# Kernel tuning notes

Measured on AMD Instinct MI355X. Metric: run time of the kernel, lower is better.

The kernel has to match this reference:

```python
import jax, jax.numpy as jnp
import numpy as np
from math import log

B, L, D = 2, 4096, 2048
H, Dh, C, KW = 16, 128, 64, 4
EPS = 1e-5
SCALE = 0.02


def setup_inputs() -> dict:
    key = jax.random.key(0)
    ks = jax.random.split(key, 16)
    rn = lambda k, shp, sc=SCALE: jax.random.normal(k, shp, jnp.float32) * sc
    # dt_bias built like the torch module
    dt = jnp.exp(jax.random.uniform(ks[7], (H,)) * (log(0.1) - log(0.001)) + log(0.001))
    dt = jnp.clip(dt, 0.0001, None)
    dt_bias = dt + jnp.log(-jnp.expm1(-dt))
    return {
        "x": jax.random.normal(ks[0], (B, L, D), jnp.float32),
        "Wq": rn(ks[1], (H * Dh, D)),
        "Wk": rn(ks[2], (H * Dh, D)),
        "Wv": rn(ks[3], (H * Dh, D)),
        "Wb": rn(ks[4], (H, D)),
        "Wa": rn(ks[5], (H, D)),
        "A_log": jnp.log(jax.random.uniform(ks[6], (H,), minval=0.01, maxval=16.0)),
        "dt_bias": dt_bias,
        "conv_q": rn(ks[8], (H * Dh, 1, KW), 0.2),
        "conv_k": rn(ks[9], (H * Dh, 1, KW), 0.2),
        "conv_v": rn(ks[10], (H * Dh, 1, KW), 0.2),
        "Wg": rn(ks[11], (H * Dh, D)),
        "norm_w": jnp.ones((Dh,), jnp.float32),
        "Wo": rn(ks[12], (D, H * Dh)),
        "S0": jnp.zeros((B, H, Dh, Dh), jnp.float32),
    }


def _causal_dwconv(x, w):
    # x: [B,L,Ch]; w: [Ch,1,KW] depthwise causal conv (left pad KW-1), then SiLU
    y = jax.lax.conv_general_dilated(
        x.transpose(0, 2, 1), w, (1,), [(KW - 1, 0)],
        feature_group_count=w.shape[0], dimension_numbers=("NCH", "OIH", "NCH"))
    return jax.nn.silu(y).transpose(0, 2, 1)


def reference(x, Wq, Wk, Wv, Wb, Wa, A_log, dt_bias, conv_q, conv_k, conv_v, Wg, norm_w, Wo, S0):
    q = _causal_dwconv(x @ Wq.T, conv_q).reshape(B, L, H, Dh).transpose(0, 2, 1, 3)  # [B,H,L,Dh]
    k = _causal_dwconv(x @ Wk.T, conv_k).reshape(B, L, H, Dh).transpose(0, 2, 1, 3)
    v = _causal_dwconv(x @ Wv.T, conv_v).reshape(B, L, H, Dh).transpose(0, 2, 1, 3)
    beta = jax.nn.sigmoid(x @ Wb.T).transpose(0, 2, 1)                                # [B,H,L]
    g = (-jnp.exp(A_log) * jax.nn.softplus(x @ Wa.T + dt_bias)).transpose(0, 2, 1)    # [B,H,L]
    l2 = lambda t: t / jnp.maximum(jnp.linalg.norm(t, axis=-1, keepdims=True), 1e-12)
    q = l2(q) / (Dh ** 0.5)
    k = l2(k)

    N = L // C  # chunks (L divisible by C)
    chop = lambda t: jnp.moveaxis(t.reshape(B, H, N, C, Dh), 2, 0)   # [N,B,H,C,Dh]
    qc, kc, vc = chop(q), chop(k), chop(v)
    betac = jnp.moveaxis(beta.reshape(B, H, N, C), 2, 0)[..., None]  # [N,B,H,C,1]
    gc = jnp.moveaxis(g.reshape(B, H, N, C), 2, 0)                   # [N,B,H,C]

    eye = jnp.eye(C, dtype=x.dtype)
    m_incl = jnp.tril(jnp.ones((C, C), bool))
    m_strict = jnp.tril(jnp.ones((C, C), bool), -1)

    def step(S, ch):
        Q, Kc, V, bet, gch = ch
        lg = jnp.cumsum(gch, axis=-1)          # log gamma, [B,H,C]
        gamma = jnp.exp(lg)
        lgC = lg[..., -1:]
        gCr = jnp.exp(lgC - lg)
        gammaC = jnp.exp(lgC)[..., None]       # [B,H,1,1]
        Qd = Q * gamma[..., None]
        Kd = gCr[..., None] * Kc
        Sd = S * gammaC
        Gam = lg[..., :, None] - lg[..., None, :]
        ratio = jnp.exp(jnp.where(m_strict, Gam, -jnp.inf))
        A = eye + bet * ratio * (Kc @ jnp.swapaxes(Kc, -1, -2))
        T = jax.scipy.linalg.solve_triangular(A, jnp.broadcast_to(eye, A.shape), lower=True)
        Wm = T @ (bet * gamma[..., None] * Kc)
        U = T @ (bet * V)
        St = jnp.swapaxes(S, -1, -2)
        GM = jnp.exp(jnp.where(m_incl, Gam, -jnp.inf))
        mid = U - Wm @ St                      # [B,H,C,Dh]
        O = Qd @ St + ((Q @ jnp.swapaxes(Kc, -1, -2)) * GM) @ mid
        S_new = Sd + jnp.swapaxes(mid, -1, -2) @ Kd
        return S_new, O

    S_fin, Os = jax.lax.scan(step, S0, (qc, kc, vc, betac, gc))
    o = Os.transpose(1, 0, 3, 2, 4).reshape(B, L, H, Dh)  # chunks -> [B,L,H,Dh]
    gate = (x @ Wg.T).reshape(B, L, H, Dh)
    # gated RMSNorm: rms-normalize o, scale by weight, gate with SiLU(g)
    o = o * jax.lax.rsqrt(jnp.mean(o * o, axis=-1, keepdims=True) + EPS) * norm_w * jax.nn.silu(gate)
    return (o.reshape(B, L, H * Dh) @ Wo.T, S_fin)
```

## Files before the change

### kernel.cpp

```cpp
#include <hip/hip_runtime.h>
#include <math.h>

#define B_   2
#define L_   4096
#define D_   2048
#define H_   16
#define DH   128
#define CH   64
#define NCH  64
#define HD   2048
#define BH   32
#define BHL  131072
#define PSZ  16777216ull

typedef unsigned short u16;
typedef __attribute__((ext_vector_type(8))) short bf16x8;
typedef __attribute__((ext_vector_type(4))) float f32x4;
#define MFMA16(a, b, c) __builtin_amdgcn_mfma_f32_16x16x32_bf16(a, b, c, 0, 0, 0)

static __device__ __forceinline__ float sigm(float x) { return 1.0f / (1.0f + expf(-x)); }

static __device__ __forceinline__ float b2f(u16 u) {
    union { float f; unsigned int i; } v; v.i = ((unsigned int)u) << 16; return v.f;
}
static __device__ __forceinline__ u16 f2b(float f) {
    union { float f; unsigned int i; } v; v.f = f;
    unsigned int r = v.i + 0x7fffu + ((v.i >> 16) & 1u);
    return (u16)(r >> 16);
}
static __device__ __forceinline__ void b8ld(const u16* p, float* d) {
    uint4 u = *(const uint4*)p;
    d[0] = b2f((u16)(u.x & 0xffff)); d[1] = b2f((u16)(u.x >> 16));
    d[2] = b2f((u16)(u.y & 0xffff)); d[3] = b2f((u16)(u.y >> 16));
    d[4] = b2f((u16)(u.z & 0xffff)); d[5] = b2f((u16)(u.z >> 16));
    d[6] = b2f((u16)(u.w & 0xffff)); d[7] = b2f((u16)(u.w >> 16));
}
static __device__ __forceinline__ void b8st(const float* s, u16* p) {
    uint4 u;
    u.x = (unsigned)f2b(s[0]) | ((unsigned)f2b(s[1]) << 16);
    u.y = (unsigned)f2b(s[2]) | ((unsigned)f2b(s[3]) << 16);
    u.z = (unsigned)f2b(s[4]) | ((unsigned)f2b(s[5]) << 16);
    u.w = (unsigned)f2b(s[6]) | ((unsigned)f2b(s[7]) << 16);
    *(uint4*)p = u;
}
static __device__ __forceinline__ float4 ldA4(const u16* p) {
    ushort4 u = *(const ushort4*)p;
    float4 f; f.x = b2f(u.x); f.y = b2f(u.y); f.z = b2f(u.z); f.w = b2f(u.w); return f;
}
static __device__ __forceinline__ void cstore(float* p, float v) { *p = v; }
static __device__ __forceinline__ void cstore(u16* p, float v) { *p = f2b(v); }

static __device__ __forceinline__ void async16(const u16* g, u16* l) {
    __builtin_amdgcn_global_load_lds(
        (const __attribute__((address_space(1))) unsigned int*)g,
        (__attribute__((address_space(3))) unsigned int*)l, 16, 0, 0);
}

__global__ __launch_bounds__(256) void cvt_f2b(const float* __restrict__ in,
                                               u16* __restrict__ out, int n8) {
    int i = blockIdx.x * 256 + threadIdx.x;
    if (i >= n8) return;
    float t[8];
    float4 a = *(const float4*)(in + (size_t)i * 8);
    float4 b = *(const float4*)(in + (size_t)i * 8 + 4);
    t[0] = a.x; t[1] = a.y; t[2] = a.z; t[3] = a.w;
    t[4] = b.x; t[5] = b.y; t[6] = b.z; t[7] = b.w;
    b8st(t, out + (size_t)i * 8);
}

template <typename TC>
__global__ __launch_bounds__(256) void gemm_bt_async(const u16* __restrict__ A,
                                                     const u16* __restrict__ Bm,
                                                     TC* __restrict__ Cm,
                                                     int M, int N, int K) {
    __shared__ __align__(16) u16 sA[128 * 64];
    __shared__ __align__(16) u16 sB[128 * 64];
    const int tid = threadIdx.x;
    const int w = tid >> 6, lane = tid & 63, lq = lane >> 4, ln = lane & 15;
    const int wm = w >> 1, wn = w & 1;
    const int mbase = blockIdx.y * 128, nbase = blockIdx.x * 128;

    f32x4 acc[4][4];
#pragma unroll
    for (int mt = 0; mt < 4; mt++)
#pragma unroll
        for (int nt = 0; nt < 4; nt++) acc[mt][nt] = (f32x4){0.f, 0.f, 0.f, 0.f};

    for (int k0 = 0; k0 < K; k0 += 64) {
#pragma unroll
        for (int j = 0; j < 4; j++) {
            int c = tid + 256 * j;
            int row = c >> 3;
            int oct = (c & 7) ^ (row & 7);
            async16(A + (size_t)(mbase + row) * K + k0 + oct * 8, &sA[c * 8]);
            async16(Bm + (size_t)(nbase + row) * K + k0 + oct * 8, &sB[c * 8]);
        }
        __syncthreads();
#pragma unroll
        for (int ks = 0; ks < 2; ks++) {
            const int o = ks * 4 + lq;
            bf16x8 af[4], bfr[4];
#pragma unroll
            for (int mt = 0; mt < 4; mt++) {
                int m = wm * 64 + mt * 16 + ln;
                af[mt] = *(const bf16x8*)&sA[(m << 6) + ((o ^ (m & 7)) << 3)];
            }
#pragma unroll
            for (int nt = 0; nt < 4; nt++) {
                int nn = wn * 64 + nt * 16 + ln;
                bfr[nt] = *(const bf16x8*)&sB[(nn << 6) + ((o ^ (nn & 7)) << 3)];
            }
#pragma unroll
            for (int mt = 0; mt < 4; mt++)
#pragma unroll
                for (int nt = 0; nt < 4; nt++)
                    acc[mt][nt] = MFMA16(af[mt], bfr[nt], acc[mt][nt]);
        }
        __syncthreads();
    }
#pragma unroll
    for (int mt = 0; mt < 4; mt++)
#pragma unroll
        for (int nt = 0; nt < 4; nt++) {
            int col = nbase + wn * 64 + nt * 16 + ln;
#pragma unroll
            for (int r = 0; r < 4; r++) {
                int row = mbase + wm * 64 + mt * 16 + lq * 4 + r;
                cstore(Cm + (size_t)row * N + col, acc[mt][nt][r]);
            }
        }
}

__global__ __launch_bounds__(256) void conv_silu_norm(const u16* __restrict__ pre,
                                                      const float* __restrict__ w,
                                                      u16* __restrict__ out, int mode) {
    int wid = blockIdx.x * 4 + (threadIdx.x >> 6);
    int lane = threadIdx.x & 63;
    int l = wid & (L_ - 1);
    int bh = wid >> 12;
    int b = bh >> 4, h = bh & 15;

    float vals[2];
    float sumsq = 0.0f;
#pragma unroll
    for (int s = 0; s < 2; s++) {
        int d = lane + 64 * s;
        int c = h * DH + d;
        const u16* col = pre + (size_t)b * L_ * HD + c;
        float acc = 0.0f;
        if (l >= 3) {
            acc = w[c * 4 + 0] * b2f(col[(size_t)(l - 3) * HD]) +
                  w[c * 4 + 1] * b2f(col[(size_t)(l - 2) * HD]) +
                  w[c * 4 + 2] * b2f(col[(size_t)(l - 1) * HD]) +
                  w[c * 4 + 3] * b2f(col[(size_t)l * HD]);
        } else {
#pragma unroll
            for (int j = 0; j < 4; j++) {
                int ll = l - 3 + j;
                if (ll >= 0) acc += w[c * 4 + j] * b2f(col[(size_t)ll * HD]);
            }
        }
        float y = acc * sigm(acc);
        vals[s] = y;
        sumsq += y * y;
    }
    if (mode < 2) {
#pragma unroll
        for (int m = 32; m >= 1; m >>= 1) sumsq += __shfl_xor(sumsq, m, 64);
        float scale = 1.0f / fmaxf(sqrtf(sumsq), 1e-12f);
        if (mode == 0) scale *= 0.08838834764831843f;
        vals[0] *= scale;
        vals[1] *= scale;
    }
    u16* o = out + ((size_t)bh * L_ + l) * DH;
    o[lane] = f2b(vals[0]);
    o[lane + 64] = f2b(vals[1]);
}

__global__ __launch_bounds__(64) void proj_small(const float* __restrict__ x,
                                                 const float* __restrict__ Wb,
                                                 const float* __restrict__ Wa,
                                                 float* __restrict__ bpre,
                                                 float* __restrict__ apre) {
    int row = blockIdx.x;
    int lane = threadIdx.x;
    const float* xr = x + (size_t)row * D_;
    float xv[32];
#pragma unroll
    for (int j = 0; j < 32; j++) xv[j] = xr[lane + 64 * j];
    for (int h = 0; h < 16; h++) {
        const float* wr = Wb + (size_t)h * D_;
        float acc = 0.0f;
#pragma unroll
        for (int j = 0; j < 32; j++) acc += xv[j] * wr[lane + 64 * j];
#pragma unroll
        for (int m = 32; m >= 1; m >>= 1) acc += __shfl_xor(acc, m, 64);
        if (lane == 0) bpre[(size_t)row * 16 + h] = acc;
    }
    for (int h = 0; h < 16; h++) {
        const float* wr = Wa + (size_t)h * D_;
        float acc = 0.0f;
#pragma unroll
        for (int j = 0; j < 32; j++) acc += xv[j] * wr[lane + 64 * j];
#pragma unroll
        for (int m = 32; m >= 1; m >>= 1) acc += __shfl_xor(acc, m, 64);
        if (lane == 0) apre[(size_t)row * 16 + h] = acc;
    }
}

__global__ __launch_bounds__(256) void beta_g_k(const float* __restrict__ bpre,
                                                const float* __restrict__ apre,
                                                const float* __restrict__ A_log,
                                                const float* __restrict__ dt_bias,
                                                float* __restrict__ beta, float* __restrict__ g) {
    int gi = blockIdx.x * 256 + threadIdx.x;
    int l = gi & (L_ - 1);
    int bh = gi >> 12;
    int b = bh >> 4, h = bh & 15;
    float bp = bpre[((size_t)b * L_ + l) * 16 + h];
    float ap = apre[((size_t)b * L_ + l) * 16 + h] + dt_bias[h];
    float sp = (ap > 20.0f) ? ap : log1pf(expf(ap));
    beta[(size_t)bh * L_ + l] = 1.0f / (1.0f + expf(-bp));
    g[(size_t)bh * L_ + l] = -expf(A_log[h]) * sp;
}

__global__ __launch_bounds__(256) void prep_chunks(u16* __restrict__ q, u16* __restrict__ k,
                                                   u16* __restrict__ v,
                                                   const float* __restrict__ beta,
                                                   const float* __restrict__ g,
                                                   u16* __restrict__ Wm, u16* __restrict__ W2,
                                                   float* __restrict__ gamC) {
    __shared__ __align__(16) u16 sKb[64 * 136];
    __shared__ __align__(16) float sA[64 * 65];
    __shared__ __align__(16) float sT[64 * 68];
    __shared__ float sLg[CH], sGam[CH], sGcr[CH], sBeta[CH];

    const int cid = blockIdx.x;
    const int bh = cid >> 6, n = cid & 63;
    const int tid = threadIdx.x;
    const int w = tid >> 6, lane = tid & 63, lq = lane >> 4, ln = lane & 15;
    const size_t cbase = ((size_t)bh * L_ + (size_t)n * CH) * DH;
    u16* qw = q + cbase;
    u16* kw = k + cbase;
    u16* vc = v + cbase;

    bf16x8 aQ[4];
    {
        const u16* qrow = qw + (size_t)(w * 16 + ln) * DH;
#pragma unroll
        for (int ks = 0; ks < 4; ks++)
            aQ[ks] = *(const bf16x8*)(qrow + ks * 32 + lq * 8);
    }
#pragma unroll
    for (int rep = 0; rep < 4; rep++) {
        int f = tid + 256 * rep;
        int row = f >> 4, c8 = (f & 15) * 8;
        *(uint4*)&sKb[row * 136 + c8] = *(const uint4*)(kw + (size_t)row * DH + c8);
    }
    if (tid < 64) {
        float lg = g[(size_t)bh * L_ + (size_t)n * CH + tid];
#pragma unroll
        for (int off = 1; off < 64; off <<= 1) {
            float u = __shfl_up(lg, off, 64);
            if (tid >= off) lg += u;
        }
        float lgC = __shfl(lg, 63, 64);
        sLg[tid] = lg;
        sGam[tid] = expf(lg);
        sGcr[tid] = expf(lgC - lg);
        sBeta[tid] = beta[(size_t)bh * L_ + (size_t)n * CH + tid];
        if (tid == 63) gamC[cid] = expf(lgC);
    }
    __syncthreads();

    {
        f32x4 accA[4], accQ[4];
#pragma unroll
        for (int nt = 0; nt < 4; nt++) {
            accA[nt] = (f32x4){0.f, 0.f, 0.f, 0.f};
            accQ[nt] = (f32x4){0.f, 0.f, 0.f, 0.f};
        }
#pragma unroll
        for (int ks = 0; ks < 4; ks++) {
            int k0 = ks * 32 + lq * 8;
            bf16x8 aK = *(const bf16x8*)&sKb[(w * 16 + ln) * 136 + k0];
#pragma unroll
            for (int nt = 0; nt < 4; nt++) {
                bf16x8 bK = *(const bf16x8*)&sKb[(nt * 16 + ln) * 136 + k0];
                accA[nt] = MFMA16(aK, bK, accA[nt]);
                accQ[nt] = MFMA16(aQ[ks], bK, accQ[nt]);
            }
        }
        for (int idx = tid; idx < 64 * 68; idx += 256) sT[idx] = 0.f;
        u16* w2c = W2 + (size_t)cid * CH * CH;
#pragma unroll
        for (int nt = 0; nt < 4; nt++) {
            int j = nt * 16 + ln;
            float lgj = sLg[j];
#pragma unroll
            for (int r = 0; r < 4; r++) {
                int i = w * 16 + lq * 4 + r;
                float dexp = expf(fminf(sLg[i] - lgj, 0.f));
                sA[i * 65 + j] = (j < i) ? sBeta[i] * dexp * accA[nt][r] : 0.f;
                w2c[i * CH + j] = f2b((j <= i) ? accQ[nt][r] * dexp : 0.f);
            }
        }
    }
    __syncthreads();

    float colv[16];
    {
        const int i0 = w * 16;
        colv[0] = (ln == 0) ? 1.f : 0.f;
#pragma unroll
        for (int i = 1; i < 16; i++) {
            float acc = (ln == i) ? 1.f : 0.f;
#pragma unroll
            for (int kk = 0; kk < 15; kk++) {
                if (kk < i) acc -= sA[(i0 + i) * 65 + i0 + kk] * colv[kk];
            }
            colv[i] = acc;
        }
    }
#pragma unroll
    for (int rep = 0; rep < 4; rep++) {
        int f = tid + 256 * rep;
        int i = f >> 4, d8 = (f & 15) * 8;
        float tq[8], tk[8];
        b8ld(qw + (size_t)i * DH + d8, tq);
        b8ld(kw + (size_t)i * DH + d8, tk);
        float sq = sGam[i], sk2 = sGcr[i];
#pragma unroll
        for (int jj = 0; jj < 8; jj++) { tq[jj] *= sq; tk[jj] *= sk2; }
        b8st(tq, qw + (size_t)i * DH + d8);
        b8st(tk, kw + (size_t)i * DH + d8);
    }
    if (lq == 0) {
#pragma unroll
        for (int i = 0; i < 16; i++) sT[(w * 16 + i) * 68 + w * 16 + ln] = colv[i];
    }
    __syncthreads();

    auto trijob = [&](int bi, int bj) {
        float accv[4] = {0.f, 0.f, 0.f, 0.f};
        for (int kb = bj; kb < bi; kb++) {
#pragma unroll
            for (int kk = 0; kk < 16; kk++) {
                float bv = sT[(kb * 16 + kk) * 68 + bj * 16 + ln];
#pragma unroll
                for (int r = 0; r < 4; r++)
                    accv[r] += sA[(bi * 16 + lq * 4 + r) * 65 + kb * 16 + kk] * bv;
            }
        }
        float xv[4] = {0.f, 0.f, 0.f, 0.f};
#pragma unroll
        for (int kk = 0; kk < 16; kk++) {
            float bv = __shfl(accv[kk & 3], (kk >> 2) * 16 + ln, 64);
#pragma unroll
            for (int r = 0; r < 4; r++)
                xv[r] -= sT[(bi * 16 + lq * 4 + r) * 68 + bi * 16 + kk] * bv;
        }
#pragma unroll
        for (int r = 0; r < 4; r++)
            sT[(bi * 16 + lq * 4 + r) * 68 + bj * 16 + ln] = xv[r];
    };
    if (w < 3) trijob(w + 1, w);
    __syncthreads();
    if (w < 2) trijob(w + 2, w);
    __syncthreads();
    if (w == 0) trijob(3, 0);
    __syncthreads();

    {
        int ib = tid >> 4, cb = tid & 15;
        int i0 = ib * 4, c0 = cb * 8;
        float accK[4][8], accV[4][8];
#pragma unroll
        for (int r = 0; r < 4; r++)
#pragma unroll
            for (int c = 0; c < 8; c++) { accK[r][c] = 0.0f; accV[r][c] = 0.0f; }
        for (int kk = 0; kk < CH; kk += 4) {
            float tr[4][4];
#pragma unroll
            for (int r = 0; r < 4; r++) {
                float4 t4 = *(const float4*)&sT[(i0 + r) * 68 + kk];
                tr[r][0] = t4.x; tr[r][1] = t4.y; tr[r][2] = t4.z; tr[r][3] = t4.w;
            }
#pragma unroll
            for (int s = 0; s < 4; s++) {
                int kks = kk + s;
                float va[8], ka[8];
                b8ld(vc + (size_t)kks * DH + c0, va);
                b8ld(&sKb[kks * 136 + c0], ka);
                float bv = sBeta[kks];
                float kf = bv * sGam[kks];
#pragma unroll
                for (int c = 0; c < 8; c++) { va[c] *= bv; ka[c] *= kf; }
#pragma unroll
                for (int r = 0; r < 4; r++) {
                    float t = tr[r][s];
#pragma unroll
                    for (int c = 0; c < 8; c++) {
                        accK[r][c] += t * ka[c];
                        accV[r][c] += t * va[c];
                    }
                }
            }
        }
        u16* wmc = Wm + (size_t)cid * CH * DH;
#pragma unroll
        for (int r = 0; r < 4; r++) b8st(&accK[r][0], wmc + (size_t)(i0 + r) * DH + c0);
        __syncthreads();
#pragma unroll
        for (int r = 0; r < 4; r++) b8st(&accV[r][0], vc + (size_t)(i0 + r) * DH + c0);
    }
}

__global__ __launch_bounds__(256) void scan_mfma(const u16* __restrict__ Wm,
                                                 const u16* __restrict__ U,
                                                 const u16* __restrict__ Qd,
                                                 const u16* __restrict__ Kd,
                                                 const u16* __restrict__ W2,
                                                 const float* __restrict__ gamC,
                                                 const float* __restrict__ S0,
                                                 float* __restrict__ Og,
                                                 float* __restrict__ Sfin) {
    __shared__ __align__(16) u16 sWm[64 * 136];
    __shared__ __align__(16) u16 sQd[64 * 136];
    __shared__ __align__(16) u16 sKdT[128 * 72];
    __shared__ __align__(16) u16 sW2[64 * 72];
    __shared__ __align__(16) u16 sS[16 * 136];
    __shared__ __align__(16) u16 sMidT[16 * 72];

    const int bid = blockIdx.x;
    const int bh = bid >> 3, dg = bid & 7, d0 = dg * 16;
    const int tid = threadIdx.x;
    const int w = tid >> 6, lane = tid & 63, lq = lane >> 4, ln = lane & 15;

    f32x4 S_t[2];
#pragma unroll
    for (int t2 = 0; t2 < 2; t2++)
#pragma unroll
        for (int r = 0; r < 4; r++)
            S_t[t2][r] = S0[(size_t)bh * DH * DH + (size_t)(d0 + lq * 4 + r) * DH + w * 32 + t2 * 16 + ln];

    for (int n = 0; n < NCH; n++) {
        const size_t cid = (size_t)bh * NCH + n;
        const u16* wmc = Wm + cid * CH * DH;
        const size_t tb = ((size_t)bh * L_ + (size_t)n * CH) * DH;
        const u16* uc = U + tb;
        const u16* qc = Qd + tb;
        const u16* kc = Kd + tb;
        const u16* w2c = W2 + cid * CH * CH;
        const float gC = gamC[cid];

#pragma unroll
        for (int t2 = 0; t2 < 2; t2++)
#pragma unroll
            for (int r = 0; r < 4; r++)
                sS[(lq * 4 + r) * 136 + w * 32 + t2 * 16 + ln] = f2b(S_t[t2][r]);

#pragma unroll
        for (int j = 0; j < 4; j++) {
            int f = tid + 256 * j;
            int row = f >> 4, kc8 = (f & 15) * 8;
            *(uint4*)&sWm[row * 136 + kc8] = *(const uint4*)(wmc + f * 8);
            *(uint4*)&sQd[row * 136 + kc8] = *(const uint4*)(qc + f * 8);
        }
#pragma unroll
        for (int j = 0; j < 2; j++) {
            int f = tid + 256 * j;
            int row = f >> 3, c8 = (f & 7) * 8;
            *(uint4*)&sW2[row * 72 + c8] = *(const uint4*)(w2c + f * 8);
        }
#pragma unroll
        for (int rep = 0; rep < 8; rep++) {
            int f = tid + 256 * rep;
            int i = f >> 5, e4 = (f & 31) * 4;
            ushort4 vv = *(const ushort4*)(kc + (size_t)f * 4);
            sKdT[(e4 + 0) * 72 + i] = vv.x;
            sKdT[(e4 + 1) * 72 + i] = vv.y;
            sKdT[(e4 + 2) * 72 + i] = vv.z;
            sKdT[(e4 + 3) * 72 + i] = vv.w;
        }
        __syncthreads();

        f32x4 macc = (f32x4){0.f, 0.f, 0.f, 0.f};
#pragma unroll
        for (int ks = 0; ks < 4; ks++) {
            bf16x8 a = *(const bf16x8*)&sWm[(w * 16 + ln) * 136 + ks * 32 + lq * 8];
            bf16x8 b = *(const bf16x8*)&sS[ln * 136 + ks * 32 + lq * 8];
            macc = MFMA16(a, b, macc);
        }
#pragma unroll
        for (int r = 0; r < 4; r++) {
            int i = w * 16 + lq * 4 + r;
            float mv = b2f(uc[(size_t)i * DH + d0 + ln]) - macc[r];
            sMidT[ln * 72 + i] = f2b(mv);
        }
        __syncthreads();

        f32x4 oacc = (f32x4){0.f, 0.f, 0.f, 0.f};
#pragma unroll
        for (int ks = 0; ks < 4; ks++) {
            bf16x8 a = *(const bf16x8*)&sQd[(w * 16 + ln) * 136 + ks * 32 + lq * 8];
            bf16x8 b = *(const bf16x8*)&sS[ln * 136 + ks * 32 + lq * 8];
            oacc = MFMA16(a, b, oacc);
        }
#pragma unroll
        for (int ks = 0; ks < 2; ks++) {
            bf16x8 a = *(const bf16x8*)&sW2[(w * 16 + ln) * 72 + ks * 32 + lq * 8];
            bf16x8 b = *(const bf16x8*)&sMidT[ln * 72 + ks * 32 + lq * 8];
            oacc = MFMA16(a, b, oacc);
        }
#pragma unroll
        for (int r = 0; r < 4; r++) {
            int i = w * 16 + lq * 4 + r;
            Og[((size_t)bh * L_ + (size_t)n * CH + i) * DH + d0 + ln] = oacc[r];
        }

#pragma unroll
        for (int t2 = 0; t2 < 2; t2++)
#pragma unroll
            for (int r = 0; r < 4; r++) S_t[t2][r] *= gC;
#pragma unroll
        for (int ks = 0; ks < 2; ks++) {
            bf16x8 a = *(const bf16x8*)&sMidT[ln * 72 + ks * 32 + lq * 8];
#pragma unroll
            for (int t2 = 0; t2 < 2; t2++) {
                bf16x8 b = *(const bf16x8*)&sKdT[((2 * w + t2) * 16 + ln) * 72 + ks * 32 + lq * 8];
                S_t[t2] = MFMA16(a, b, S_t[t2]);
            }
        }
        __syncthreads();
    }

#pragma unroll
    for (int t2 = 0; t2 < 2; t2++)
#pragma unroll
        for (int r = 0; r < 4; r++)
            Sfin[(size_t)bh * DH * DH + (size_t)(d0 + lq * 4 + r) * DH + w * 32 + t2 * 16 + ln] = S_t[t2][r];
}

__global__ __launch_bounds__(256) void epilogue_gate(const float* __restrict__ Ob,
                                                     const u16* __restrict__ gpre,
                                                     const float* __restrict__ norm_w,
                                                     u16* __restrict__ gated) {
    int wid = blockIdx.x * 4 + (threadIdx.x >> 6);
    int lane = threadIdx.x & 63;
    int l = wid & (L_ - 1);
    int bh = wid >> 12;
    int b = bh >> 4, h = bh & 15;
    const float* orow = Ob + ((size_t)bh * L_ + l) * DH;
    float o0 = orow[lane], o1 = orow[lane + 64];
    float ss = o0 * o0 + o1 * o1;
#pragma unroll
    for (int m = 32; m >= 1; m >>= 1) ss += __shfl_xor(ss, m, 64);
    float r = rsqrtf(ss * (1.0f / 128.0f) + 1e-5f);
    size_t gidx = ((size_t)b * L_ + l) * HD + h * DH;
    float gp0 = b2f(gpre[gidx + lane]), gp1 = b2f(gpre[gidx + lane + 64]);
    gated[gidx + lane] = f2b(o0 * r * norm_w[lane] * (gp0 * sigm(gp0)));
    gated[gidx + lane + 64] = f2b(o1 * r * norm_w[lane + 64] * (gp1 * sigm(gp1)));
}

extern "C" void kernel_launch(void* const* d_in, const int* in_sizes, int n_in,
                              void* d_out, int out_size, void* d_ws, size_t ws_size,
                              hipStream_t stream) {
    const float* x       = (const float*)d_in[0];
    const float* Wq      = (const float*)d_in[1];
    const float* Wk      = (const float*)d_in[2];
    const float* Wv      = (const float*)d_in[3];
    const float* Wb      = (const float*)d_in[4];
    const float* Wa      = (const float*)d_in[5];
    const float* A_log   = (const float*)d_in[6];
    const float* dt_bias = (const float*)d_in[7];
    const float* conv_q  = (const float*)d_in[8];
    const float* conv_k  = (const float*)d_in[9];
    const float* conv_v  = (const float*)d_in[10];
    const float* Wg      = (const float*)d_in[11];
    const float* norm_w  = (const float*)d_in[12];
    const float* Wo      = (const float*)d_in[13];
    const float* S0      = (const float*)d_in[14];
    float* out = (float*)d_out;

    u16* Pb = (u16*)d_ws;
    u16* Qb = Pb + PSZ;
    u16* Kb = Qb + PSZ;
    u16* Vb = Kb + PSZ;
    u16* W2b = Vb + PSZ;
    u16* xb  = W2b + PSZ / 2;
    u16* wbuf = xb + PSZ;
    float* bpre = (float*)(wbuf + 4194304);
    float* apre = bpre + BHL;
    float* betab = apre + BHL;
    float* gbuf = betab + BHL;
    float* gamC = gbuf + BHL;

    float* Obuf = out;
    float* Sfin = out + PSZ;

    dim3 gblk(16, 64);
    const int W8 = 2048 * 2048 / 8;

    cvt_f2b<<<8192, 256, 0, stream>>>(x, xb, (int)(PSZ / 8));
    cvt_f2b<<<2048, 256, 0, stream>>>(Wq, wbuf, W8);
    gemm_bt_async<u16><<<gblk, 256, 0, stream>>>(xb, wbuf, Pb, 8192, 2048, 2048);
    conv_silu_norm<<<32768, 256, 0, stream>>>(Pb, conv_q, Qb, 0);
    cvt_f2b<<<2048, 256, 0, stream>>>(Wk, wbuf, W8);
    gemm_bt_async<u16><<<gblk, 256, 0, stream>>>(xb, wbuf, Pb, 8192, 2048, 2048);
    conv_silu_norm<<<32768, 256, 0, stream>>>(Pb, conv_k, Kb, 1);
    cvt_f2b<<<2048, 256, 0, stream>>>(Wv, wbuf, W8);
    gemm_bt_async<u16><<<gblk, 256, 0, stream>>>(xb, wbuf, Pb, 8192, 2048, 2048);
    conv_silu_norm<<<32768, 256, 0, stream>>>(Pb, conv_v, Vb, 2);
    proj_small<<<8192, 64, 0, stream>>>(x, Wb, Wa, bpre, apre);
    beta_g_k<<<512, 256, 0, stream>>>(bpre, apre, A_log, dt_bias, betab, gbuf);
    prep_chunks<<<2048, 256, 0, stream>>>(Qb, Kb, Vb, betab, gbuf, Pb, W2b, gamC);
    scan_mfma<<<256, 256, 0, stream>>>(Pb, Vb, Qb, Kb, W2b, gamC, S0, Obuf, Sfin);
    cvt_f2b<<<2048, 256, 0, stream>>>(Wg, wbuf, W8);
    gemm_bt_async<u16><<<gblk, 256, 0, stream>>>(xb, wbuf, Vb, 8192, 2048, 2048);
    epilogue_gate<<<32768, 256, 0, stream>>>(Obuf, Vb, norm_w, Kb);
    cvt_f2b<<<2048, 256, 0, stream>>>(Wo, wbuf, W8);
    gemm_bt_async<float><<<gblk, 256, 0, stream>>>(Kb, wbuf, out, 8192, 2048, 2048);
}
```

Baseline: 1.189 ms.

## Double-buffer scan chunk loads with async global-to-LDS copies and swizzled layouts

The sequential chunk scan now prefetches the next chunk's Wm, Qd and W2 tiles into a second LDS buffer using global_load_lds, and holds Kd, U and the decay in registers while the current chunk computes. This hides global-memory latency on the serial recurrence path. Padded LDS rows are replaced with XOR-swizzled layouts so the async copies can write contiguous lines. Blocks are also remapped so heads spread across XCDs. It uses twice the LDS, which may cut occupancy, and relies on hand-placed waitcnt and barrier calls for correctness.

```diff
diff --git a/kernel.cpp b/kernel.cpp
--- a/kernel.cpp
+++ b/kernel.cpp
@@ -43,10 +43,6 @@
     u.w = (unsigned)f2b(s[6]) | ((unsigned)f2b(s[7]) << 16);
     *(uint4*)p = u;
 }
-static __device__ __forceinline__ float4 ldA4(const u16* p) {
-    ushort4 u = *(const ushort4*)p;
-    float4 f; f.x = b2f(u.x); f.y = b2f(u.y); f.z = b2f(u.z); f.w = b2f(u.w); return f;
-}
 static __device__ __forceinline__ void cstore(float* p, float v) { *p = v; }
 static __device__ __forceinline__ void cstore(u16* p, float v) { *p = f2b(v); }
 
@@ -54,6 +50,17 @@
     __builtin_amdgcn_global_load_lds(
         (const __attribute__((address_space(1))) unsigned int*)g,
         (__attribute__((address_space(3))) unsigned int*)l, 16, 0, 0);
+}
+
+static __device__ __forceinline__ void bar_lgkm() {
+    asm volatile("s_waitcnt lgkmcnt(0)" ::: "memory");
+    __builtin_amdgcn_sched_barrier(0);
+    __builtin_amdgcn_s_barrier();
+    __builtin_amdgcn_sched_barrier(0);
+}
+static __device__ __forceinline__ void wait_vm0() {
+    asm volatile("s_waitcnt vmcnt(0)" ::: "memory");
+    __builtin_amdgcn_sched_barrier(0);
 }
 
 __global__ __launch_bounds__(256) void cvt_f2b(const float* __restrict__ in,
@@ -425,15 +432,16 @@
                                                  const float* __restrict__ S0,
                                                  float* __restrict__ Og,
                                                  float* __restrict__ Sfin) {
-    __shared__ __align__(16) u16 sWm[64 * 136];
-    __shared__ __align__(16) u16 sQd[64 * 136];
-    __shared__ __align__(16) u16 sKdT[128 * 72];
-    __shared__ __align__(16) u16 sW2[64 * 72];
-    __shared__ __align__(16) u16 sS[16 * 136];
+    __shared__ __align__(16) u16 sWm[2][64 * 128];
+    __shared__ __align__(16) u16 sQd[2][64 * 128];
+    __shared__ __align__(16) u16 sW2[2][64 * 64];
+    __shared__ __align__(16) u16 sKdT[2][128 * 64];
+    __shared__ __align__(16) u16 sS[2][16 * 136];
     __shared__ __align__(16) u16 sMidT[16 * 72];
 
     const int bid = blockIdx.x;
-    const int bh = bid >> 3, dg = bid & 7, d0 = dg * 16;
+    const int xcd = bid & 7, slot = bid >> 3;
+    const int bh = xcd + 8 * (slot >> 3), dg = slot & 7, d0 = dg * 16;
     const int tid = threadIdx.x;
     const int w = tid >> 6, lane = tid & 63, lq = lane >> 4, ln = lane & 15;
 
@@ -444,95 +452,151 @@
         for (int r = 0; r < 4; r++)
             S_t[t2][r] = S0[(size_t)bh * DH * DH + (size_t)(d0 + lq * 4 + r) * DH + w * 32 + t2 * 16 + ln];
 
-    for (int n = 0; n < NCH; n++) {
-        const size_t cid = (size_t)bh * NCH + n;
-        const u16* wmc = Wm + cid * CH * DH;
-        const size_t tb = ((size_t)bh * L_ + (size_t)n * CH) * DH;
-        const u16* uc = U + tb;
-        const u16* qc = Qd + tb;
-        const u16* kc = Kd + tb;
-        const u16* w2c = W2 + cid * CH * CH;
-        const float gC = gamC[cid];
-
-#pragma unroll
-        for (int t2 = 0; t2 < 2; t2++)
-#pragma unroll
-            for (int r = 0; r < 4; r++)
-                sS[(lq * 4 + r) * 136 + w * 32 + t2 * 16 + ln] = f2b(S_t[t2][r]);
-
+    auto stage_async = [&](int m, int p) {
+        const size_t cid2 = (size_t)bh * NCH + m;
+        const u16* wmc = Wm + cid2 * CH * DH;
+        const u16* qc  = Qd + ((size_t)bh * L_ + (size_t)m * CH) * DH;
+        const u16* w2c = W2 + cid2 * CH * CH;
 #pragma unroll
         for (int j = 0; j < 4; j++) {
-            int f = tid + 256 * j;
-            int row = f >> 4, kc8 = (f & 15) * 8;
-            *(uint4*)&sWm[row * 136 + kc8] = *(const uint4*)(wmc + f * 8);
-            *(uint4*)&sQd[row * 136 + kc8] = *(const uint4*)(qc + f * 8);
+            int c = tid + 256 * j;
+            int row = c >> 4;
+            int osrc = (c & 15) ^ (row & 7);
+            async16(wmc + (size_t)row * DH + osrc * 8, &sWm[p][c * 8]);
+            async16(qc  + (size_t)row * DH + osrc * 8, &sQd[p][c * 8]);
         }
 #pragma unroll
         for (int j = 0; j < 2; j++) {
-            int f = tid + 256 * j;
-            int row = f >> 3, c8 = (f & 7) * 8;
-            *(uint4*)&sW2[row * 72 + c8] = *(const uint4*)(w2c + f * 8);
-        }
+            int c = tid + 256 * j;
+            int row = c >> 3;
+            int osrc = (c & 7) ^ (row & 7);
+            async16(w2c + (size_t)row * CH + osrc * 8, &sW2[p][c * 8]);
+        }
+    };
+    ushort4 kreg[8];
+    auto load_kreg = [&](int m) {
+        const u16* kc = Kd + ((size_t)bh * L_ + (size_t)m * CH) * DH;
+#pragma unroll
+        for (int rep = 0; rep < 8; rep++)
+            kreg[rep] = *(const ushort4*)(kc + (size_t)(tid + 256 * rep) * 4);
+    };
+    auto write_kdt = [&](int p) {
 #pragma unroll
         for (int rep = 0; rep < 8; rep++) {
             int f = tid + 256 * rep;
             int i = f >> 5, e4 = (f & 31) * 4;
-            ushort4 vv = *(const ushort4*)(kc + (size_t)f * 4);
-            sKdT[(e4 + 0) * 72 + i] = vv.x;
-            sKdT[(e4 + 1) * 72 + i] = vv.y;
-            sKdT[(e4 + 2) * 72 + i] = vv.z;
-            sKdT[(e4 + 3) * 72 + i] = vv.w;
-        }
-        __syncthreads();
-
-        f32x4 macc = (f32x4){0.f, 0.f, 0.f, 0.f};
-#pragma unroll
-        for (int ks = 0; ks < 4; ks++) {
-            bf16x8 a = *(const bf16x8*)&sWm[(w * 16 + ln) * 136 + ks * 32 + lq * 8];
-            bf16x8 b = *(const bf16x8*)&sS[ln * 136 + ks * 32 + lq * 8];
-            macc = MFMA16(a, b, macc);
-        }
-#pragma unroll
-        for (int r = 0; r < 4; r++) {
-            int i = w * 16 + lq * 4 + r;
-            float mv = b2f(uc[(size_t)i * DH + d0 + ln]) - macc[r];
-            sMidT[ln * 72 + i] = f2b(mv);
-        }
-        __syncthreads();
-
-        f32x4 oacc = (f32x4){0.f, 0.f, 0.f, 0.f};
-#pragma unroll
-        for (int ks = 0; ks < 4; ks++) {
-            bf16x8 a = *(const bf16x8*)&sQd[(w * 16 + ln) * 136 + ks * 32 + lq * 8];
-            bf16x8 b = *(const bf16x8*)&sS[ln * 136 + ks * 32 + lq * 8];
-            oacc = MFMA16(a, b, oacc);
-        }
-#pragma unroll
-        for (int ks = 0; ks < 2; ks++) {
-            bf16x8 a = *(const bf16x8*)&sW2[(w * 16 + ln) * 72 + ks * 32 + lq * 8];
-            bf16x8 b = *(const bf16x8*)&sMidT[ln * 72 + ks * 32 + lq * 8];
-            oacc = MFMA16(a, b, oacc);
-        }
-#pragma unroll
-        for (int r = 0; r < 4; r++) {
-            int i = w * 16 + lq * 4 + r;
-            Og[((size_t)bh * L_ + (size_t)n * CH + i) * DH + d0 + ln] = oacc[r];
-        }
-
+            int io = i >> 3, il = i & 7;
+            ushort4 vv = kreg[rep];
+            sKdT[p][(e4 + 0) * 64 + ((io ^ ((e4 + 0) & 7)) << 3) + il] = vv.x;
+            sKdT[p][(e4 + 1) * 64 + ((io ^ ((e4 + 1) & 7)) << 3) + il] = vv.y;
+            sKdT[p][(e4 + 2) * 64 + ((io ^ ((e4 + 2) & 7)) << 3) + il] = vv.z;
+            sKdT[p][(e4 + 3) * 64 + ((io ^ ((e4 + 3) & 7)) << 3) + il] = vv.w;
+        }
+    };
+    auto write_ss = [&](int p) {
 #pragma unroll
         for (int t2 = 0; t2 < 2; t2++)
 #pragma unroll
-            for (int r = 0; r < 4; r++) S_t[t2][r] *= gC;
+            for (int r = 0; r < 4; r++)
+                sS[p][(lq * 4 + r) * 136 + w * 32 + t2 * 16 + ln] = f2b(S_t[t2][r]);
+    };
+
+    u16 ureg[4], uregN[4];
+    auto load_ureg = [&](int m, u16* dst) {
+        const u16* uc = U + ((size_t)bh * L_ + (size_t)m * CH) * DH;
+#pragma unroll
+        for (int r = 0; r < 4; r++)
+            dst[r] = uc[(size_t)(w * 16 + lq * 4 + r) * DH + d0 + ln];
+    };
+
+    stage_async(0, 0);
+    load_kreg(0);
+    load_ureg(0, ureg);
+    float gCur = gamC[(size_t)bh * NCH];
+    float gNext = 0.f;
+    wait_vm0();
+    write_kdt(0);
+    write_ss(0);
+    bar_lgkm();
+
+    for (int n = 0; n < NCH; n++) {
+        const int p = n & 1;
+        const bool hasN = (n + 1 < NCH);
+        if (hasN) {
+            stage_async(n + 1, p ^ 1);
+            load_kreg(n + 1);
+            load_ureg(n + 1, uregN);
+            gNext = gamC[(size_t)bh * NCH + n + 1];
+        }
+
+        {
+            f32x4 macc = (f32x4){0.f, 0.f, 0.f, 0.f};
+            const int i = w * 16 + ln;
+#pragma unroll
+            for (int ks = 0; ks < 4; ks++) {
+                int o = ks * 4 + lq;
+                bf16x8 a = *(const bf16x8*)&sWm[p][i * 128 + ((o ^ (i & 7)) << 3)];
+                bf16x8 b = *(const bf16x8*)&sS[p][ln * 136 + ks * 32 + lq * 8];
+                macc = MFMA16(a, b, macc);
+            }
+#pragma unroll
+            for (int r = 0; r < 4; r++) {
+                int ii = w * 16 + lq * 4 + r;
+                float mv = b2f(ureg[r]) - macc[r];
+                sMidT[ln * 72 + ii] = f2b(mv);
+            }
+        }
+        bar_lgkm();
+
+        {
+            f32x4 oacc = (f32x4){0.f, 0.f, 0.f, 0.f};
+            const int i = w * 16 + ln;
+#pragma unroll
+            for (int ks = 0; ks < 4; ks++) {
+                int o = ks * 4 + lq;
+                bf16x8 a = *(const bf16x8*)&sQd[p][i * 128 + ((o ^ (i & 7)) << 3)];
+                bf16x8 b = *(const bf16x8*)&sS[p][ln * 136 + ks * 32 + lq * 8];
+                oacc = MFMA16(a, b, oacc);
+            }
+#pragma unroll
+            for (int ks = 0; ks < 2; ks++) {
+                int o = ks * 4 + lq;
+                bf16x8 a = *(const bf16x8*)&sW2[p][i * 64 + ((o ^ (i & 7)) << 3)];
+                bf16x8 b = *(const bf16x8*)&sMidT[ln * 72 + ks * 32 + lq * 8];
+                oacc = MFMA16(a, b, oacc);
+            }
+#pragma unroll
+            for (int r = 0; r < 4; r++) {
+                int ii = w * 16 + lq * 4 + r;
+                Og[((size_t)bh * L_ + (size_t)n * CH + ii) * DH + d0 + ln] = oacc[r];
+            }
+        }
+
+#pragma unroll
+        for (int t2 = 0; t2 < 2; t2++)
+#pragma unroll
+            for (int r = 0; r < 4; r++) S_t[t2][r] *= gCur;
 #pragma unroll
         for (int ks = 0; ks < 2; ks++) {
             bf16x8 a = *(const bf16x8*)&sMidT[ln * 72 + ks * 32 + lq * 8];
 #pragma unroll
             for (int t2 = 0; t2 < 2; t2++) {
-                bf16x8 b = *(const bf16x8*)&sKdT[((2 * w + t2) * 16 + ln) * 72 + ks * 32 + lq * 8];
+                int e = (2 * w + t2) * 16 + ln;
+                int o = ks * 4 + lq;
+                bf16x8 b = *(const bf16x8*)&sKdT[p][e * 64 + ((o ^ (e & 7)) << 3)];
                 S_t[t2] = MFMA16(a, b, S_t[t2]);
             }
         }
-        __syncthreads();
+
+        if (hasN) {
+            wait_vm0();
+            write_kdt(p ^ 1);
+            write_ss(p ^ 1);
+#pragma unroll
+            for (int r = 0; r < 4; r++) ureg[r] = uregN[r];
+            gCur = gNext;
+            bar_lgkm();
+        }
     }
 
 #pragma unroll
```

After: 1.195 ms. Within noise of the previous version (+0.5%).
